# Kernel optimization log

Measured on AMD Instinct MI355X. Metric: run time of the kernel, lower is better.

## Reference

```python
import jax, jax.numpy as jnp
import numpy as np

MARGIN = 1.0  # init kwarg margin
EPS = 1e-16


def setup_inputs() -> dict:
    key = jax.random.key(0)
    k1, k2 = jax.random.split(key)
    embeddings = jax.random.normal(k1, (512, 128), dtype=jnp.float32)
    labels = jax.random.randint(k2, (512,), 0, 32)
    return {"embeddings": embeddings, "labels": labels}


def _pairwise_l2(e):
    # exact p=2 cdist via explicit differences; safe sqrt so grad at d=0 is 0
    diff = e[:, None, :] - e[None, :, :]          # [N, N, D]
    sq = jnp.sum(diff * diff, axis=-1)             # [N, N]
    safe = jnp.where(sq > 0, sq, 1.0)
    return jnp.where(sq > 0, jnp.sqrt(safe), 0.0)


def reference(embeddings, labels):
    # _batch_all_triplet_loss (default mining_type='online_hard_negative')
    n = labels.shape[0]
    d = _pairwise_l2(embeddings)                   # [N, N]

    not_eye = ~jnp.eye(n, dtype=bool)
    # distinct (i, j, k) triplets
    distinct = not_eye[:, :, None] & not_eye[:, None, :] & not_eye[None, :, :]
    label_eq = labels[:, None] == labels[None, :]  # symmetric [N, N]
    # labels[i] == labels[j] and labels[i] != labels[k]
    mask = label_eq[:, :, None] & (~label_eq[:, None, :]) & distinct  # [N, N, N]

    # d(a, p) - d(a, n) + margin, masked and hinged
    triplet_loss = mask.astype(d.dtype) * (d[:, :, None] - d[:, None, :] + MARGIN)
    triplet_loss = jnp.maximum(triplet_loss, 0.0)

    n_positive = jnp.sum(triplet_loss > EPS).astype(d.dtype)
    n_triplets = jnp.sum(mask).astype(d.dtype)
    fraction_positive = n_positive / (n_triplets + EPS)
    loss = jnp.sum(triplet_loss) / (n_positive + EPS)
    return loss, fraction_positive
```

## Files before the change

kernel.cpp:

```cpp
#include <hip/hip_runtime.h>

constexpr int N = 512;
constexpr int D = 128;
constexpr int A = 2;
constexpr int NBLK = N / A;
constexpr float MARGIN = 1.0f;
constexpr float EPS_T = 1e-16f;

__global__ __launch_bounds__(512) void triplet_main_k(
    const float* __restrict__ emb, const int* __restrict__ labels,
    double* __restrict__ partial)
{
    __shared__ float  drow[A][N];
    __shared__ float  posd[A][128];
    __shared__ int    cnt[A][8];
    __shared__ int    npos_s[A];
    __shared__ double red[24];

    const int i0   = blockIdx.x * A;
    const int tid  = threadIdx.x;
    const int lane = tid & 63;
    const int wid  = tid >> 6;
    const int sub4 = tid & 3;

    const float4* ea0 = reinterpret_cast<const float4*>(emb + (size_t)i0 * D);
    const float4* ea1 = reinterpret_cast<const float4*>(emb + (size_t)(i0 + 1) * D);
    float4 A0[8], A1[8];
    #pragma unroll
    for (int c = 0; c < 8; ++c) { A0[c] = ea0[sub4 + 4 * c]; A1[c] = ea1[sub4 + 4 * c]; }

    const int lk  = labels[tid];
    const int li0 = labels[i0];
    const int li1 = labels[i0 + 1];

    #pragma unroll 2
    for (int p = 0; p < 4; ++p) {
        const int r = p * 128 + (tid >> 2);
        const float4* er = reinterpret_cast<const float4*>(emb + (size_t)r * D);
        float4 V[8];
        #pragma unroll
        for (int c = 0; c < 8; ++c) V[c] = er[sub4 + 4 * c];
        float sq0 = 0.f, sq1 = 0.f;
        #pragma unroll
        for (int c = 0; c < 8; ++c) {
            float d0 = A0[c].x - V[c].x, d1 = A0[c].y - V[c].y;
            float d2 = A0[c].z - V[c].z, d3 = A0[c].w - V[c].w;
            sq0 += d0 * d0 + d1 * d1 + d2 * d2 + d3 * d3;
            d0 = A1[c].x - V[c].x; d1 = A1[c].y - V[c].y;
            d2 = A1[c].z - V[c].z; d3 = A1[c].w - V[c].w;
            sq1 += d0 * d0 + d1 * d1 + d2 * d2 + d3 * d3;
        }
        sq0 += __shfl_xor(sq0, 1); sq1 += __shfl_xor(sq1, 1);
        sq0 += __shfl_xor(sq0, 2); sq1 += __shfl_xor(sq1, 2);
        if (sub4 == 0) {
            drow[0][r] = (sq0 > 0.f) ? sqrtf(sq0) : 0.f;
            drow[1][r] = (sq1 > 0.f) ? sqrtf(sq1) : 0.f;
        }
    }
    __syncthreads();

    const int j = tid;
    const bool p0 = (labels[j] == li0) && (j != i0);
    const bool p1 = (labels[j] == li1) && (j != i0 + 1);
    const unsigned long long m0 = __ballot(p0);
    const unsigned long long m1 = __ballot(p1);
    if (lane == 0) { cnt[0][wid] = __popcll(m0); cnt[1][wid] = __popcll(m1); }
    __syncthreads();
    int base0 = 0, base1 = 0;
    #pragma unroll
    for (int w = 0; w < 8; ++w) {
        base0 += (w < wid) ? cnt[0][w] : 0;
        base1 += (w < wid) ? cnt[1][w] : 0;
    }
    const unsigned long long lm = (1ull << lane) - 1ull;
    if (p0) posd[0][base0 + __popcll(m0 & lm)] = drow[0][j];
    if (p1) posd[1][base1 + __popcll(m1 & lm)] = drow[1][j];
    if (tid == 0) {
        int t0 = 0, t1 = 0;
        #pragma unroll
        for (int w = 0; w < 8; ++w) { t0 += cnt[0][w]; t1 += cnt[1][w]; }
        npos_s[0] = t0; npos_s[1] = t1;
    }
    __syncthreads();

    double sum = 0.0;
    int np_i = 0, nt_i = 0;
    {
        const float dik = drow[0][tid];
        if (lk != li0) {
            const int npos = npos_s[0];
            for (int p = 0; p < npos; ++p) {
                const float t = (posd[0][p] - dik) + MARGIN;
                if (t > EPS_T) { sum += (double)t; ++np_i; }
            }
            nt_i += npos;
        }
    }
    {
        const float dik = drow[1][tid];
        if (lk != li1) {
            const int npos = npos_s[1];
            for (int p = 0; p < npos; ++p) {
                const float t = (posd[1][p] - dik) + MARGIN;
                if (t > EPS_T) { sum += (double)t; ++np_i; }
            }
            nt_i += npos;
        }
    }

    double s = sum, p = (double)np_i, t = (double)nt_i;
    #pragma unroll
    for (int off = 32; off > 0; off >>= 1) {
        s += __shfl_down(s, off);
        p += __shfl_down(p, off);
        t += __shfl_down(t, off);
    }
    if (lane == 0) { red[wid] = s; red[8 + wid] = p; red[16 + wid] = t; }
    __syncthreads();
    if (tid == 0) {
        double S = 0.0, P = 0.0, T = 0.0;
        #pragma unroll
        for (int w = 0; w < 8; ++w) { S += red[w]; P += red[8 + w]; T += red[16 + w]; }
        partial[4 * blockIdx.x + 0] = S;
        partial[4 * blockIdx.x + 1] = P;
        partial[4 * blockIdx.x + 2] = T;
    }
}

__global__ __launch_bounds__(64) void triplet_final_k(
    const double* __restrict__ partial, float* __restrict__ out)
{
    const int lane = threadIdx.x;
    double a = 0.0, b = 0.0, c = 0.0;
    #pragma unroll
    for (int bk = lane; bk < NBLK; bk += 64) {
        a += partial[4 * bk + 0];
        b += partial[4 * bk + 1];
        c += partial[4 * bk + 2];
    }
    #pragma unroll
    for (int off = 32; off > 0; off >>= 1) {
        a += __shfl_down(a, off);
        b += __shfl_down(b, off);
        c += __shfl_down(c, off);
    }
    if (lane == 0) {
        out[0] = (float)(a / (b + 1e-16));
        out[1] = (float)(b / (c + 1e-16));
    }
}

extern "C" void kernel_launch(void* const* d_in, const int* in_sizes, int n_in,
                              void* d_out, int out_size, void* d_ws, size_t ws_size,
                              hipStream_t stream) {
    const float* emb   = (const float*)d_in[0];
    const int*   lab   = (const int*)d_in[1];
    float*       out   = (float*)d_out;
    double*      parts = (double*)d_ws;

    triplet_main_k<<<NBLK, 512, 0, stream>>>(emb, lab, parts);
    triplet_final_k<<<1, 64, 0, stream>>>(parts, out);
}
```

Baseline: 15.17 us.

## Precompute positive compaction indices and write per-wave partials to drop block barriers

```diff
diff --git a/kernel.cpp b/kernel.cpp
--- a/kernel.cpp
+++ b/kernel.cpp
@@ -11,11 +11,11 @@
     const float* __restrict__ emb, const int* __restrict__ labels,
     double* __restrict__ partial)
 {
-    __shared__ float  drow[A][N];
-    __shared__ float  posd[A][128];
-    __shared__ int    cnt[A][8];
-    __shared__ int    npos_s[A];
-    __shared__ double red[24];
+    __shared__ float drow[A][N];
+    __shared__ float posd[A][128];
+    __shared__ int   pinv[A][N];
+    __shared__ int   cnt[A][8];
+    __shared__ int   npos_s[A];
 
     const int i0   = blockIdx.x * A;
     const int tid  = threadIdx.x;
@@ -32,6 +32,29 @@
     const int lk  = labels[tid];
     const int li0 = labels[i0];
     const int li1 = labels[i0 + 1];
+
+    const bool p0 = (lk == li0) && (tid != i0);
+    const bool p1 = (lk == li1) && (tid != i0 + 1);
+    const unsigned long long m0 = __ballot(p0);
+    const unsigned long long m1 = __ballot(p1);
+    if (lane == 0) { cnt[0][wid] = __popcll(m0); cnt[1][wid] = __popcll(m1); }
+    __syncthreads();
+    int base0 = 0, base1 = 0;
+    #pragma unroll
+    for (int w = 0; w < 8; ++w) {
+        base0 += (w < wid) ? cnt[0][w] : 0;
+        base1 += (w < wid) ? cnt[1][w] : 0;
+    }
+    const unsigned long long lm = (1ull << lane) - 1ull;
+    pinv[0][tid] = p0 ? (base0 + __popcll(m0 & lm)) : -1;
+    pinv[1][tid] = p1 ? (base1 + __popcll(m1 & lm)) : -1;
+    if (tid == 0) {
+        int t0 = 0, t1 = 0;
+        #pragma unroll
+        for (int w = 0; w < 8; ++w) { t0 += cnt[0][w]; t1 += cnt[1][w]; }
+        npos_s[0] = t0; npos_s[1] = t1;
+    }
+    __syncthreads();
 
     #pragma unroll 2
     for (int p = 0; p < 4; ++p) {
@@ -53,33 +76,15 @@
         sq0 += __shfl_xor(sq0, 1); sq1 += __shfl_xor(sq1, 1);
         sq0 += __shfl_xor(sq0, 2); sq1 += __shfl_xor(sq1, 2);
         if (sub4 == 0) {
-            drow[0][r] = (sq0 > 0.f) ? sqrtf(sq0) : 0.f;
-            drow[1][r] = (sq1 > 0.f) ? sqrtf(sq1) : 0.f;
+            const float dv0 = (sq0 > 0.f) ? sqrtf(sq0) : 0.f;
+            const float dv1 = (sq1 > 0.f) ? sqrtf(sq1) : 0.f;
+            drow[0][r] = dv0;
+            drow[1][r] = dv1;
+            const int q0 = pinv[0][r];
+            const int q1 = pinv[1][r];
+            if (q0 >= 0) posd[0][q0] = dv0;
+            if (q1 >= 0) posd[1][q1] = dv1;
         }
-    }
-    __syncthreads();
-
-    const int j = tid;
-    const bool p0 = (labels[j] == li0) && (j != i0);
-    const bool p1 = (labels[j] == li1) && (j != i0 + 1);
-    const unsigned long long m0 = __ballot(p0);
-    const unsigned long long m1 = __ballot(p1);
-    if (lane == 0) { cnt[0][wid] = __popcll(m0); cnt[1][wid] = __popcll(m1); }
-    __syncthreads();
-    int base0 = 0, base1 = 0;
-    #pragma unroll
-    for (int w = 0; w < 8; ++w) {
-        base0 += (w < wid) ? cnt[0][w] : 0;
-        base1 += (w < wid) ? cnt[1][w] : 0;
-    }
-    const unsigned long long lm = (1ull << lane) - 1ull;
-    if (p0) posd[0][base0 + __popcll(m0 & lm)] = drow[0][j];
-    if (p1) posd[1][base1 + __popcll(m1 & lm)] = drow[1][j];
-    if (tid == 0) {
-        int t0 = 0, t1 = 0;
-        #pragma unroll
-        for (int w = 0; w < 8; ++w) { t0 += cnt[0][w]; t1 += cnt[1][w]; }
-        npos_s[0] = t0; npos_s[1] = t1;
     }
     __syncthreads();
 
@@ -115,15 +120,11 @@
         p += __shfl_down(p, off);
         t += __shfl_down(t, off);
     }
-    if (lane == 0) { red[wid] = s; red[8 + wid] = p; red[16 + wid] = t; }
-    __syncthreads();
-    if (tid == 0) {
-        double S = 0.0, P = 0.0, T = 0.0;
-        #pragma unroll
-        for (int w = 0; w < 8; ++w) { S += red[w]; P += red[8 + w]; T += red[16 + w]; }
-        partial[4 * blockIdx.x + 0] = S;
-        partial[4 * blockIdx.x + 1] = P;
-        partial[4 * blockIdx.x + 2] = T;
+    if (lane == 0) {
+        const int slot = (blockIdx.x << 3) | wid;
+        partial[4 * slot + 0] = s;
+        partial[4 * slot + 1] = p;
+        partial[4 * slot + 2] = t;
     }
 }
 
@@ -132,11 +133,10 @@
 {
     const int lane = threadIdx.x;
     double a = 0.0, b = 0.0, c = 0.0;
-    #pragma unroll
-    for (int bk = lane; bk < NBLK; bk += 64) {
-        a += partial[4 * bk + 0];
-        b += partial[4 * bk + 1];
-        c += partial[4 * bk + 2];
+    for (int e = lane; e < NBLK * 8; e += 64) {
+        a += partial[4 * e + 0];
+        b += partial[4 * e + 1];
+        c += partial[4 * e + 2];
     }
     #pragma unroll
     for (int off = 32; off > 0; off >>= 1) {
```

New measurement: 22.19 us. 1.46x slower.
